# Optimization experiments

Measured on AMD Instinct MI355X. Metric: run time of the kernel, lower is better.

## Reference

```python
import jax, jax.numpy as jnp
import numpy as np
from jax import lax

V, E, T, F, K = 100000, 300, 50, 100, 3
B, S = 32, 512


def setup_inputs() -> dict:
    key = jax.random.key(0)
    ks = jax.random.split(key, 10)
    inp = {
        "x": jax.random.randint(ks[0], (B, S), 0, V),
        "tags": jax.random.randint(ks[1], (B, S), 0, T),
        "emb": jax.random.normal(ks[2], (V, E), dtype=jnp.float32),
        "conv_w": jax.random.normal(ks[3], (F, E, K), dtype=jnp.float32) / np.sqrt(E * K),
        "conv_b": jnp.zeros((F,), dtype=jnp.float32),
        "fc_w": jax.random.normal(ks[4], (T, F), dtype=jnp.float32) / np.sqrt(F),
        "fc_b": jnp.zeros((T,), dtype=jnp.float32),
        "start_trans": jax.random.uniform(ks[5], (T,), dtype=jnp.float32, minval=-0.1, maxval=0.1),
        "end_trans": jax.random.uniform(ks[6], (T,), dtype=jnp.float32, minval=-0.1, maxval=0.1),
        "trans": jax.random.uniform(ks[7], (T, T), dtype=jnp.float32, minval=-0.1, maxval=0.1),
    }
    return inp


def _emissions(x, emb, conv_w, conv_b, fc_w, fc_b):
    e = emb[x]                                   # [B,S,E] embedding gather
    e = jnp.transpose(e, (0, 2, 1))              # [B,E,S]
    h = lax.conv_general_dilated(e, conv_w, (1,), [(K // 2, K // 2)])  # [B,F,S] (NCW/OIW)
    h = jax.nn.relu(h + conv_b[None, :, None])   # dropout is identity in eval
    feat = jnp.transpose(h, (0, 2, 1))           # [B,S,F]
    return (jnp.einsum("bsf,tf->bst", feat, fc_w) + fc_b).astype(jnp.float32)  # [B,S,T]


def _crf_nll(emissions, tags, start_trans, end_trans, trans):
    # numerator: score of the gold tag path (full mask)
    em_tag = jnp.take_along_axis(emissions, tags[..., None], axis=-1)[..., 0]  # [B,S]
    num = (start_trans[tags[:, 0]]
           + em_tag.sum(-1)
           + trans[tags[:, :-1], tags[:, 1:]].sum(-1)
           + end_trans[tags[:, -1]])                                           # [B]

    # denominator: forward algorithm via scan over time
    alpha0 = start_trans[None, :] + emissions[:, 0]                             # [B,T]

    def step(alpha, em_t):
        # alpha: [B,T] prev scores; em_t: [B,T] emissions at t
        new = jax.nn.logsumexp(alpha[:, :, None] + trans[None] + em_t[:, None, :], axis=1)
        return new, None

    alpha, _ = lax.scan(step, alpha0, jnp.transpose(emissions[:, 1:], (1, 0, 2)))
    log_z = jax.nn.logsumexp(alpha + end_trans[None, :], axis=-1)               # [B]
    return -(num - log_z).sum()  # torchcrf default reduction='sum'; model returns -llh


def reference(x, tags, emb, conv_w, conv_b, fc_w, fc_b, start_trans, end_trans, trans):
    emissions = _emissions(x, emb, conv_w, conv_b, fc_w, fc_b)
    return _crf_nll(emissions, tags, start_trans, end_trans, trans)
```

## Files before the change

kernel.cpp:

```cpp
#include <hip/hip_runtime.h>
#include <hip/hip_bf16.h>
#include <math.h>

#define BB 32
#define SS 512
#define EE 300
#define FF 100
#define TT 50
#define CH 16
#define NC 32

typedef __attribute__((ext_vector_type(8))) short v8s;
typedef __attribute__((ext_vector_type(4))) float v4f;
#define MFMA16 __builtin_amdgcn_mfma_f32_16x16x32_bf16

#define AP 328
#define NCH 10
#define CKS 3
#define CHB (128 * 96)
#define A2P 136
#define MP 72

__device__ inline unsigned short f2bf(float v) {
    unsigned u = __float_as_uint(v);
    unsigned r = u + 0x7fff + ((u >> 16) & 1);
    return (unsigned short)(r >> 16);
}
__device__ inline float bf2f(short s) {
    return __uint_as_float(((unsigned)(unsigned short)s) << 16);
}
__device__ inline unsigned pkbf2(float a, float b) {
    __hip_bfloat162 h = __float22bfloat162_rn(make_float2(a, b));
    return *(unsigned*)&h;
}
__device__ inline v8s ldsld8(const short* p) {
    return *(const v8s*)__builtin_assume_aligned(p, 16);
}
__device__ inline void g2lds16(const void* g, void* l) {
    __builtin_amdgcn_global_load_lds(
        (const __attribute__((address_space(1))) unsigned int*)g,
        (__attribute__((address_space(3))) unsigned int*)l, 16, 0, 0);
}

__global__ void prep_kernel(const float* __restrict__ tr, const float* __restrict__ cw,
                            const float* __restrict__ fcw,
                            unsigned short* __restrict__ wB2,
                            unsigned short* __restrict__ fcwT2,
                            unsigned short* __restrict__ AT,
                            unsigned short* __restrict__ Ab,
                            float* __restrict__ accum, unsigned* __restrict__ cnt)
{
    const int gid = blockIdx.x * 256 + threadIdx.x;
    const int gs  = 64 * 256;
    if (gid == 0) { *accum = 0.f; *cnt = 0u; }
    for (int idx = gid; idx < NCH * CKS * 8 * 512; idx += gs) {
        int e = idx & 7, p = (idx >> 3) & 63, blk = idx >> 9;
        int ch = blk / 24, rem = blk - ch * 24;
        int sl = rem >> 3, ft = rem & 7;
        int col = p >> 2, q = p & 3;
        int n  = ft * 16 + col;
        int gk = ch * 96 + sl * 32 + q * 8 + e;
        int kk = gk / 320, ee = gk - kk * 320;
        float v = (n < FF && ee < EE) ? cw[n * 900 + ee * 3 + kk] : 0.f;
        wB2[idx] = f2bf(v);
    }
    for (int idx = gid; idx < 16 * 512; idx += gs) {
        int e = idx & 7, p = (idx >> 3) & 63, blk = idx >> 9;
        int ks = blk >> 2, nt = blk & 3;
        int col = p >> 2, q = p & 3;
        int t = nt * 16 + col, f = ks * 32 + q * 8 + e;
        float v = (t < TT && f < FF) ? fcw[t * FF + f] : 0.f;
        fcwT2[idx] = f2bf(v);
    }
    for (int idx = gid; idx < 64 * 64; idx += gs) {
        int r = idx >> 6, c2 = idx & 63;
        AT[idx] = (r < TT && c2 < TT) ? f2bf(__expf(tr[c2 * TT + r])) : 0;
        Ab[idx] = (r < TT && c2 < TT) ? f2bf(__expf(tr[r * TT + c2])) : 0;
    }
}

__global__ __launch_bounds__(256, 3) void emis_kernel(
    const int* __restrict__ x, const float* __restrict__ emb,
    const unsigned short* __restrict__ wB2, const float* __restrict__ cb,
    const unsigned short* __restrict__ fcwT2, const float* __restrict__ fcb,
    const int* __restrict__ tags,
    float* __restrict__ expem, float* __restrict__ rmv, float* __restrict__ emtag)
{
    __shared__ __align__(16) short ldsA[34 * AP];
    __shared__ __align__(16) short ldsB[CHB];

    const int b    = blockIdx.y;
    const int s0   = blockIdx.x * 32;
    const int tid  = threadIdx.x;
    const int wv   = tid >> 6;
    const int lane = tid & 63;
    const int col  = lane & 15;
    const int q    = lane >> 4;
    const int bofs = ((col << 2) | q) << 3;

#pragma unroll
    for (int it = 0; it < 6; ++it) {
        int seg = it * 4 + wv;
        g2lds16((const char*)wB2 + seg * 1024 + lane * 16,
                (char*)ldsB + seg * 1024);
    }

    int   xr[10], ofs[10], e0a[10];
#pragma unroll
    for (int it = 0; it < 10; ++it) {
        int g = tid + it * 256;
        int r = g / 75, eg = g - r * 75;
        int e0 = eg * 4;
        int src = s0 - 1 + r;
        bool v = (g < 2550) && (src >= 0) && (src < SS);
        xr[it]  = v ? x[b * SS + src] : -1;
        ofs[it] = r * AP + e0;
        e0a[it] = e0;
    }
    float4 vv[10];
#pragma unroll
    for (int it = 0; it < 10; ++it)
        vv[it] = (xr[it] >= 0)
               ? *(const float4*)(emb + (size_t)xr[it] * EE + e0a[it])
               : make_float4(0.f, 0.f, 0.f, 0.f);
#pragma unroll
    for (int it = 0; it < 10; ++it) {
        int g = tid + it * 256;
        if (g < 2550) {
            unsigned lo = pkbf2(vv[it].x, vv[it].y);
            unsigned hi = pkbf2(vv[it].z, vv[it].w);
            *(uint2*)&ldsA[ofs[it]] = make_uint2(lo, hi);
        }
    }
    if (tid < 34 * 5) {
        int r = tid / 5, c0 = 300 + (tid % 5) * 4;
        *(short4*)&ldsA[r * AP + c0] = make_short4(0, 0, 0, 0);
    }

    v4f acc[2][2];
#pragma unroll
    for (int a = 0; a < 2; ++a)
#pragma unroll
        for (int f = 0; f < 2; ++f) acc[a][f] = (v4f){0.f, 0.f, 0.f, 0.f};

    const int ftA = wv * 2, ftB = wv * 2 + 1;
    for (int ch = 0; ch < NCH; ++ch) {
        __syncthreads();
#pragma unroll
        for (int sl = 0; sl < CKS; ++sl) {
            int gk = ch * 96 + sl * 32;
            int kk = (gk >= 640) ? 2 : (gk >= 320 ? 1 : 0);
            int e0 = gk - kk * 320;
            v8s a0 = ldsld8(&ldsA[(col + kk) * AP + e0 + q * 8]);
            v8s a1 = ldsld8(&ldsA[(16 + col + kk) * AP + e0 + q * 8]);
            v8s b0 = ldsld8(&ldsB[((sl * 8 + ftA) << 9) + bofs]);
            v8s b1 = ldsld8(&ldsB[((sl * 8 + ftB) << 9) + bofs]);
            acc[0][0] = MFMA16(a0, b0, acc[0][0], 0, 0, 0);
            acc[0][1] = MFMA16(a0, b1, acc[0][1], 0, 0, 0);
            acc[1][0] = MFMA16(a1, b0, acc[1][0], 0, 0, 0);
            acc[1][1] = MFMA16(a1, b1, acc[1][1], 0, 0, 0);
        }
        __syncthreads();
        if (ch < NCH - 1) {
            const char* g = (const char*)(wB2 + (size_t)(ch + 1) * CHB);
#pragma unroll
            for (int it = 0; it < 6; ++it) {
                int seg = it * 4 + wv;
                g2lds16(g + seg * 1024 + lane * 16, (char*)ldsB + seg * 1024);
            }
        }
    }

    short* A2 = ldsA;
    short* B2 = ldsB;
#pragma unroll
    for (int it = 0; it < 4; ++it) {
        int seg = it * 4 + wv;
        g2lds16((const char*)fcwT2 + seg * 1024 + lane * 16,
                (char*)B2 + seg * 1024);
    }
#pragma unroll
    for (int st = 0; st < 2; ++st)
#pragma unroll
        for (int fi = 0; fi < 2; ++fi) {
            int f = (wv * 2 + fi) * 16 + col;
            float bias = (f < FF) ? cb[f] : 0.f;
#pragma unroll
            for (int rg = 0; rg < 4; ++rg) {
                int s = st * 16 + q * 4 + rg;
                float v = (f < FF) ? fmaxf(acc[st][fi][rg] + bias, 0.f) : 0.f;
                A2[s * A2P + f] = (short)f2bf(v);
            }
        }
    __syncthreads();

    if (wv < 2) {
        v4f a2[4];
#pragma unroll
        for (int nt = 0; nt < 4; ++nt) a2[nt] = (v4f){0.f, 0.f, 0.f, 0.f};
#pragma unroll
        for (int ks = 0; ks < 4; ++ks) {
            v8s af = ldsld8(&A2[(wv * 16 + col) * A2P + ks * 32 + q * 8]);
#pragma unroll
            for (int nt = 0; nt < 4; ++nt) {
                v8s bt = ldsld8(&B2[((ks * 4 + nt) << 9) + bofs]);
                a2[nt] = MFMA16(af, bt, a2[nt], 0, 0, 0);
            }
        }
        float fb0 = fcb[col], fb1 = fcb[16 + col], fb2 = fcb[32 + col];
        float fb3 = (col < 2) ? fcb[48 + col] : 0.f;
#pragma unroll
        for (int rg = 0; rg < 4; ++rg) {
            int s = s0 + wv * 16 + q * 4 + rg;
            float e0v = a2[0][rg] + fb0;
            float e1v = a2[1][rg] + fb1;
            float e2v = a2[2][rg] + fb2;
            float e3v = (col < 2) ? a2[3][rg] + fb3 : -1e30f;
            float m = fmaxf(fmaxf(e0v, e1v), fmaxf(e2v, e3v));
#pragma unroll
            for (int off = 1; off < 16; off <<= 1) m = fmaxf(m, __shfl_xor(m, off));
            int gidx = b * SS + s;
            if (col == 0) rmv[gidx] = m;
            int tg = tags[gidx];
            float* orow = expem + (size_t)gidx * TT;
            orow[col]      = __expf(e0v - m);
            orow[16 + col] = __expf(e1v - m);
            orow[32 + col] = __expf(e2v - m);
            if (col < 2) orow[48 + col] = __expf(e3v - m);
            if (tg == col)            emtag[gidx] = e0v;
            else if (tg == 16 + col)  emtag[gidx] = e1v;
            else if (tg == 32 + col)  emtag[gidx] = e2v;
            else if (col < 2 && tg == 48 + col) emtag[gidx] = e3v;
        }
    }
}

__global__ __launch_bounds__(64) void chunk_kernel(
    const float* __restrict__ expem, const unsigned short* __restrict__ AT,
    const unsigned short* __restrict__ Ab,
    unsigned short* __restrict__ R, float* __restrict__ lsR)
{
    __shared__ __align__(16) short L[2][64 * MP];
    __shared__ __align__(16) float emL[CH][64];
    const int c = blockIdx.x, b = blockIdx.y;
    const int lane = threadIdx.x;
    const int col = lane & 15, q = lane >> 4;
    const int t0 = c * CH + 1;
    const int nf = (c == NC - 1) ? (SS - 1 - (NC - 1) * CH) : CH;

    for (int idx = lane; idx < CH * 64; idx += 64) {
        int k = idx >> 6, m = idx & 63;
        float v = 0.f;
        if (m < TT && k < nf) v = expem[((size_t)(b * SS + t0 + k)) * TT + m];
        emL[k][m] = v;
    }

    v8s af[4][2];
#pragma unroll
    for (int jt = 0; jt < 4; ++jt)
#pragma unroll
        for (int kc = 0; kc < 2; ++kc)
            af[jt][kc] = *(const v8s*)(AT + (jt * 16 + col) * 64 + kc * 32 + q * 8);
    __syncthreads();

    {
        const v8s* arow = (const v8s*)(Ab + lane * 64);
#pragma unroll
        for (int g = 0; g < 8; ++g) {
            v8s a = arow[g];
            float f[8];
#pragma unroll
            for (int e = 0; e < 8; ++e) f[e] = bf2f(a[e]) * emL[0][g * 8 + e];
            uint4 o = make_uint4(pkbf2(f[0], f[1]), pkbf2(f[2], f[3]),
                                 pkbf2(f[4], f[5]), pkbf2(f[6], f[7]));
            *(uint4*)&L[0][lane * MP + g * 8] = o;
        }
    }

    int cur = 0;
    for (int k = 1; k < nf; ++k) {
        __syncthreads();
        v8s bf[4][2];
#pragma unroll
        for (int nt = 0; nt < 4; ++nt)
#pragma unroll
            for (int kc = 0; kc < 2; ++kc)
                bf[nt][kc] = ldsld8(&L[cur][(nt * 16 + col) * MP + kc * 32 + q * 8]);
        v4f acc[4][4];
#pragma unroll
        for (int jt = 0; jt < 4; ++jt)
#pragma unroll
            for (int nt = 0; nt < 4; ++nt) {
                acc[jt][nt] = (v4f){0.f, 0.f, 0.f, 0.f};
                acc[jt][nt] = MFMA16(af[jt][0], bf[nt][0], acc[jt][nt], 0, 0, 0);
                acc[jt][nt] = MFMA16(af[jt][1], bf[nt][1], acc[jt][nt], 0, 0, 0);
            }
        if (k < nf - 1) {
#pragma unroll
            for (int jt = 0; jt < 4; ++jt) {
                const float4 em4 = *(const float4*)&emL[k][jt * 16 + q * 4];
#pragma unroll
                for (int nt = 0; nt < 4; ++nt) {
                    uint2 o = make_uint2(
                        pkbf2(acc[jt][nt][0] * em4.x, acc[jt][nt][1] * em4.y),
                        pkbf2(acc[jt][nt][2] * em4.z, acc[jt][nt][3] * em4.w));
                    *(uint2*)&L[cur ^ 1][(nt * 16 + col) * MP + jt * 16 + q * 4] = o;
                }
            }
            cur ^= 1;
        } else {
            float vals[4][4][4];
            float mx = 0.f;
#pragma unroll
            for (int jt = 0; jt < 4; ++jt) {
                const float4 em4 = *(const float4*)&emL[k][jt * 16 + q * 4];
#pragma unroll
                for (int nt = 0; nt < 4; ++nt) {
                    vals[jt][nt][0] = acc[jt][nt][0] * em4.x;
                    vals[jt][nt][1] = acc[jt][nt][1] * em4.y;
                    vals[jt][nt][2] = acc[jt][nt][2] * em4.z;
                    vals[jt][nt][3] = acc[jt][nt][3] * em4.w;
#pragma unroll
                    for (int r = 0; r < 4; ++r) mx = fmaxf(mx, vals[jt][nt][r]);
                }
            }
#pragma unroll
            for (int off = 1; off < 64; off <<= 1) mx = fmaxf(mx, __shfl_xor(mx, off));
            mx = fmaxf(mx, 1e-37f);
            float inv = 1.f / mx;
            unsigned short* Rc = R + ((size_t)(b * NC + c) << 12);
#pragma unroll
            for (int jt = 0; jt < 4; ++jt)
#pragma unroll
                for (int nt = 0; nt < 4; ++nt)
#pragma unroll
                    for (int r = 0; r < 4; ++r)
                        Rc[(jt * 16 + q * 4 + r) * 64 + nt * 16 + col] =
                            f2bf(vals[jt][nt][r] * inv);
            if (lane == 0) lsR[b * NC + c] = __logf(mx);
        }
    }
}

__global__ __launch_bounds__(256) void chain_kernel(
    const float* __restrict__ expem, const unsigned short* __restrict__ R,
    const float* __restrict__ lsR, const float* __restrict__ start,
    const float* __restrict__ endt,
    const float* __restrict__ emtag, const float* __restrict__ rmv,
    const int* __restrict__ tags, const float* __restrict__ tr,
    float* __restrict__ accum, unsigned* __restrict__ cnt,
    float* __restrict__ out)
{
    __shared__ __align__(16) float pvec[64];
    __shared__ float red[8];
    __shared__ float lzsh;
    const int b = blockIdx.x, tid = threadIdx.x;
    const int wv = tid >> 6, i = tid & 63;

    if (wv == 0) {
        pvec[i] = (i < TT) ? __expf(start[i]) * expem[((size_t)(b * SS)) * TT + i] : 0.f;
        const unsigned short* Rb = R + ((size_t)(b * NC) << 12);
        v8s rb[3][8];
#pragma unroll
        for (int pc = 0; pc < 3; ++pc)
#pragma unroll
            for (int g = 0; g < 8; ++g)
                rb[pc][g] = *(const v8s*)(Rb + ((size_t)pc << 12) + i * 64 + g * 8);
        float logacc = 0.f;
#pragma unroll
        for (int c = 0; c < NC; ++c) {
            const int slot = c % 3;
            float acc = 0.f;
            const float4* pv = (const float4*)pvec;
#pragma unroll
            for (int g = 0; g < 8; ++g) {
                v8s v = rb[slot][g];
                float4 pA = pv[g * 2], pB = pv[g * 2 + 1];
                acc = fmaf(bf2f(v[0]), pA.x, acc);
                acc = fmaf(bf2f(v[1]), pA.y, acc);
                acc = fmaf(bf2f(v[2]), pA.z, acc);
                acc = fmaf(bf2f(v[3]), pA.w, acc);
                acc = fmaf(bf2f(v[4]), pB.x, acc);
                acc = fmaf(bf2f(v[5]), pB.y, acc);
                acc = fmaf(bf2f(v[6]), pB.z, acc);
                acc = fmaf(bf2f(v[7]), pB.w, acc);
            }
            if (c + 3 < NC) {
                const unsigned short* Rn = Rb + ((size_t)(c + 3) << 12);
#pragma unroll
                for (int g = 0; g < 8; ++g)
                    rb[slot][g] = *(const v8s*)(Rn + i * 64 + g * 8);
            }
            float mx = acc;
#pragma unroll
            for (int off = 1; off < 64; off <<= 1) mx = fmaxf(mx, __shfl_xor(mx, off));
            mx = fmaxf(mx, 1e-37f);
            logacc += __logf(mx) + lsR[b * NC + c];
            pvec[i] = acc * (1.f / mx);
        }
        float sv = (i < TT) ? pvec[i] * __expf(endt[i]) : 0.f;
#pragma unroll
        for (int off = 1; off < 64; off <<= 1) sv += __shfl_xor(sv, off);
        if (i == 0) lzsh = logacc + __logf(sv);
    } else {
        float accN = 0.f, accR = 0.f;
        for (int s = tid - 64; s < SS; s += 192) {
            int gi = b * SS + s;
            accN += emtag[gi];
            accR += rmv[gi];
            int tg = tags[gi];
            if (s < SS - 1) accN += tr[tg * TT + tags[gi + 1]];
        }
#pragma unroll
        for (int off = 1; off < 64; off <<= 1) {
            accN += __shfl_xor(accN, off);
            accR += __shfl_xor(accR, off);
        }
        if (i == 0) { red[wv] = accN; red[4 + wv] = accR; }
    }
    __syncthreads();
    if (tid == 0) {
        float tn  = red[1] + red[2] + red[3];
        float trm = red[5] + red[6] + red[7];
        float num = tn + start[tags[b * SS]] + endt[tags[b * SS + SS - 1]];
        float nll = trm + lzsh - num;
        atomicAdd(accum, nll);
        __threadfence();
        unsigned old = atomicAdd(cnt, 1u);
        if (old == BB - 1) out[0] = atomicAdd(accum, 0.f);
    }
}

extern "C" void kernel_launch(void* const* d_in, const int* in_sizes, int n_in,
                              void* d_out, int out_size, void* d_ws, size_t ws_size,
                              hipStream_t stream)
{
    const int*   x    = (const int*)d_in[0];
    const int*   tags = (const int*)d_in[1];
    const float* emb  = (const float*)d_in[2];
    const float* cw   = (const float*)d_in[3];
    const float* cb   = (const float*)d_in[4];
    const float* fcw  = (const float*)d_in[5];
    const float* fcb  = (const float*)d_in[6];
    const float* st   = (const float*)d_in[7];
    const float* en   = (const float*)d_in[8];
    const float* tr   = (const float*)d_in[9];

    unsigned short* wB2   = (unsigned short*)d_ws;
    unsigned short* fcwT2 = wB2 + NCH * CKS * 8 * 512;
    unsigned short* ATm   = fcwT2 + 16 * 512;
    unsigned short* Abm   = ATm + 4096;
    unsigned short* Rm    = Abm + 4096;
    float* fbase   = (float*)(Rm + (size_t)BB * NC * 4096);
    float* expem   = fbase;
    float* rmv     = expem + (size_t)BB * SS * TT;
    float* emtag   = rmv + BB * SS;
    float* lsR     = emtag + BB * SS;
    float* accum   = lsR + BB * NC;
    unsigned* cnt  = (unsigned*)(accum + 1);

    prep_kernel<<<dim3(64), 256, 0, stream>>>(tr, cw, fcw, wB2, fcwT2, ATm, Abm,
                                              accum, cnt);
    emis_kernel<<<dim3(16, BB), 256, 0, stream>>>(x, emb, wB2, cb, fcwT2, fcb,
                                                  tags, expem, rmv, emtag);
    chunk_kernel<<<dim3(NC, BB), 64, 0, stream>>>(expem, ATm, Abm, Rm, lsR);
    chain_kernel<<<dim3(BB), 256, 0, stream>>>(expem, Rm, lsR, st, en,
                                               emtag, rmv, tags, tr,
                                               accum, cnt, (float*)d_out);
}
```

Measured before the change: 241.4 us.

## Fuse chunk and chain kernels via last-block detection; fold numerator into emission kernel

Merges the per-chunk transfer-matrix kernel and the sequential chain kernel into one launch. The last chunk block to finish for each batch, detected with a per-batch atomic counter, runs the forward-chain reduction. The gold-path numerator and the row-max correction are now summed into a per-batch partial inside the emission kernel, which removes the rmv/emtag buffers and their re-read. The chunk kernel also moves to two waves per block, each handling half the output rows, and the chain uses four-deep prefetch with split accumulators. This removes one launch and some global traffic, but adds atomics, fences and an extra barrier for the cross-wave max.

```diff
diff --git a/kernel.cpp b/kernel.cpp
--- a/kernel.cpp
+++ b/kernel.cpp
@@ -48,11 +48,13 @@
                             unsigned short* __restrict__ fcwT2,
                             unsigned short* __restrict__ AT,
                             unsigned short* __restrict__ Ab,
-                            float* __restrict__ accum, unsigned* __restrict__ cnt)
+                            float* __restrict__ accum, unsigned* __restrict__ cnt,
+                            float* __restrict__ nllpart, unsigned* __restrict__ doneb)
 {
     const int gid = blockIdx.x * 256 + threadIdx.x;
     const int gs  = 64 * 256;
     if (gid == 0) { *accum = 0.f; *cnt = 0u; }
+    if (gid < BB) { nllpart[gid] = 0.f; doneb[gid] = 0u; }
     for (int idx = gid; idx < NCH * CKS * 8 * 512; idx += gs) {
         int e = idx & 7, p = (idx >> 3) & 63, blk = idx >> 9;
         int ch = blk / 24, rem = blk - ch * 24;
@@ -83,11 +85,13 @@
     const int* __restrict__ x, const float* __restrict__ emb,
     const unsigned short* __restrict__ wB2, const float* __restrict__ cb,
     const unsigned short* __restrict__ fcwT2, const float* __restrict__ fcb,
-    const int* __restrict__ tags,
-    float* __restrict__ expem, float* __restrict__ rmv, float* __restrict__ emtag)
+    const int* __restrict__ tags, const float* __restrict__ tr,
+    const float* __restrict__ start, const float* __restrict__ endt,
+    float* __restrict__ expem, float* __restrict__ nllpart)
 {
     __shared__ __align__(16) short ldsA[34 * AP];
     __shared__ __align__(16) short ldsB[CHB];
+    __shared__ float redN[2];
 
     const int b    = blockIdx.y;
     const int s0   = blockIdx.x * 32;
@@ -209,6 +213,7 @@
         }
         float fb0 = fcb[col], fb1 = fcb[16 + col], fb2 = fcb[32 + col];
         float fb3 = (col < 2) ? fcb[48 + col] : 0.f;
+        float nllp = 0.f;
 #pragma unroll
         for (int rg = 0; rg < 4; ++rg) {
             int s = s0 + wv * 16 + q * 4 + rg;
@@ -220,60 +225,80 @@
 #pragma unroll
             for (int off = 1; off < 16; off <<= 1) m = fmaxf(m, __shfl_xor(m, off));
             int gidx = b * SS + s;
-            if (col == 0) rmv[gidx] = m;
             int tg = tags[gidx];
             float* orow = expem + (size_t)gidx * TT;
             orow[col]      = __expf(e0v - m);
             orow[16 + col] = __expf(e1v - m);
             orow[32 + col] = __expf(e2v - m);
             if (col < 2) orow[48 + col] = __expf(e3v - m);
-            if (tg == col)            emtag[gidx] = e0v;
-            else if (tg == 16 + col)  emtag[gidx] = e1v;
-            else if (tg == 32 + col)  emtag[gidx] = e2v;
-            else if (col < 2 && tg == 48 + col) emtag[gidx] = e3v;
-        }
-    }
-}
-
-__global__ __launch_bounds__(64) void chunk_kernel(
+            if (tg == col)            nllp -= e0v;
+            else if (tg == 16 + col)  nllp -= e1v;
+            else if (tg == 32 + col)  nllp -= e2v;
+            else if (col < 2 && tg == 48 + col) nllp -= e3v;
+            if (col == 0) {
+                nllp += m;
+                if (s < SS - 1) nllp -= tr[tg * TT + tags[gidx + 1]];
+                if (s == 0)      nllp -= start[tg];
+                if (s == SS - 1) nllp -= endt[tg];
+            }
+        }
+#pragma unroll
+        for (int off = 1; off < 64; off <<= 1) nllp += __shfl_xor(nllp, off);
+        if (lane == 0) redN[wv] = nllp;
+    }
+    __syncthreads();
+    if (tid == 0) atomicAdd(nllpart + b, redN[0] + redN[1]);
+}
+
+__global__ __launch_bounds__(128) void chunkchain_kernel(
     const float* __restrict__ expem, const unsigned short* __restrict__ AT,
     const unsigned short* __restrict__ Ab,
-    unsigned short* __restrict__ R, float* __restrict__ lsR)
+    unsigned short* __restrict__ R, float* __restrict__ lsR,
+    const float* __restrict__ start, const float* __restrict__ endt,
+    const float* __restrict__ nllpart, unsigned* __restrict__ doneb,
+    float* __restrict__ accum, unsigned* __restrict__ cnt,
+    float* __restrict__ out)
 {
     __shared__ __align__(16) short L[2][64 * MP];
     __shared__ __align__(16) float emL[CH][64];
+    __shared__ float mxsh[2];
+    __shared__ unsigned lastf;
     const int c = blockIdx.x, b = blockIdx.y;
-    const int lane = threadIdx.x;
+    const int tid  = threadIdx.x;
+    const int wv   = tid >> 6;
+    const int lane = tid & 63;
     const int col = lane & 15, q = lane >> 4;
     const int t0 = c * CH + 1;
     const int nf = (c == NC - 1) ? (SS - 1 - (NC - 1) * CH) : CH;
 
-    for (int idx = lane; idx < CH * 64; idx += 64) {
+    for (int idx = tid; idx < CH * 64; idx += 128) {
         int k = idx >> 6, m = idx & 63;
         float v = 0.f;
         if (m < TT && k < nf) v = expem[((size_t)(b * SS + t0 + k)) * TT + m];
         emL[k][m] = v;
     }
 
-    v8s af[4][2];
-#pragma unroll
-    for (int jt = 0; jt < 4; ++jt)
+    v8s af[2][2];
+#pragma unroll
+    for (int jl = 0; jl < 2; ++jl)
 #pragma unroll
         for (int kc = 0; kc < 2; ++kc)
-            af[jt][kc] = *(const v8s*)(AT + (jt * 16 + col) * 64 + kc * 32 + q * 8);
+            af[jl][kc] = *(const v8s*)(AT + ((wv * 2 + jl) * 16 + col) * 64 + kc * 32 + q * 8);
     __syncthreads();
 
     {
-        const v8s* arow = (const v8s*)(Ab + lane * 64);
-#pragma unroll
-        for (int g = 0; g < 8; ++g) {
+        const int row = tid >> 1, half = tid & 1;
+        const v8s* arow = (const v8s*)(Ab + row * 64);
+#pragma unroll
+        for (int gh = 0; gh < 4; ++gh) {
+            int g = half * 4 + gh;
             v8s a = arow[g];
             float f[8];
 #pragma unroll
             for (int e = 0; e < 8; ++e) f[e] = bf2f(a[e]) * emL[0][g * 8 + e];
             uint4 o = make_uint4(pkbf2(f[0], f[1]), pkbf2(f[2], f[3]),
                                  pkbf2(f[4], f[5]), pkbf2(f[6], f[7]));
-            *(uint4*)&L[0][lane * MP + g * 8] = o;
+            *(uint4*)&L[0][row * MP + g * 8] = o;
         }
     }
 
@@ -286,148 +311,130 @@
 #pragma unroll
             for (int kc = 0; kc < 2; ++kc)
                 bf[nt][kc] = ldsld8(&L[cur][(nt * 16 + col) * MP + kc * 32 + q * 8]);
-        v4f acc[4][4];
-#pragma unroll
-        for (int jt = 0; jt < 4; ++jt)
+        v4f acc[2][4];
+#pragma unroll
+        for (int jl = 0; jl < 2; ++jl)
 #pragma unroll
             for (int nt = 0; nt < 4; ++nt) {
-                acc[jt][nt] = (v4f){0.f, 0.f, 0.f, 0.f};
-                acc[jt][nt] = MFMA16(af[jt][0], bf[nt][0], acc[jt][nt], 0, 0, 0);
-                acc[jt][nt] = MFMA16(af[jt][1], bf[nt][1], acc[jt][nt], 0, 0, 0);
+                acc[jl][nt] = (v4f){0.f, 0.f, 0.f, 0.f};
+                acc[jl][nt] = MFMA16(af[jl][0], bf[nt][0], acc[jl][nt], 0, 0, 0);
+                acc[jl][nt] = MFMA16(af[jl][1], bf[nt][1], acc[jl][nt], 0, 0, 0);
             }
         if (k < nf - 1) {
 #pragma unroll
-            for (int jt = 0; jt < 4; ++jt) {
+            for (int jl = 0; jl < 2; ++jl) {
+                const int jt = wv * 2 + jl;
                 const float4 em4 = *(const float4*)&emL[k][jt * 16 + q * 4];
 #pragma unroll
                 for (int nt = 0; nt < 4; ++nt) {
                     uint2 o = make_uint2(
-                        pkbf2(acc[jt][nt][0] * em4.x, acc[jt][nt][1] * em4.y),
-                        pkbf2(acc[jt][nt][2] * em4.z, acc[jt][nt][3] * em4.w));
+                        pkbf2(acc[jl][nt][0] * em4.x, acc[jl][nt][1] * em4.y),
+                        pkbf2(acc[jl][nt][2] * em4.z, acc[jl][nt][3] * em4.w));
                     *(uint2*)&L[cur ^ 1][(nt * 16 + col) * MP + jt * 16 + q * 4] = o;
                 }
             }
             cur ^= 1;
         } else {
-            float vals[4][4][4];
+            float vals[2][4][4];
             float mx = 0.f;
 #pragma unroll
-            for (int jt = 0; jt < 4; ++jt) {
+            for (int jl = 0; jl < 2; ++jl) {
+                const int jt = wv * 2 + jl;
                 const float4 em4 = *(const float4*)&emL[k][jt * 16 + q * 4];
 #pragma unroll
                 for (int nt = 0; nt < 4; ++nt) {
-                    vals[jt][nt][0] = acc[jt][nt][0] * em4.x;
-                    vals[jt][nt][1] = acc[jt][nt][1] * em4.y;
-                    vals[jt][nt][2] = acc[jt][nt][2] * em4.z;
-                    vals[jt][nt][3] = acc[jt][nt][3] * em4.w;
-#pragma unroll
-                    for (int r = 0; r < 4; ++r) mx = fmaxf(mx, vals[jt][nt][r]);
+                    vals[jl][nt][0] = acc[jl][nt][0] * em4.x;
+                    vals[jl][nt][1] = acc[jl][nt][1] * em4.y;
+                    vals[jl][nt][2] = acc[jl][nt][2] * em4.z;
+                    vals[jl][nt][3] = acc[jl][nt][3] * em4.w;
+#pragma unroll
+                    for (int r = 0; r < 4; ++r) mx = fmaxf(mx, vals[jl][nt][r]);
                 }
             }
 #pragma unroll
             for (int off = 1; off < 64; off <<= 1) mx = fmaxf(mx, __shfl_xor(mx, off));
-            mx = fmaxf(mx, 1e-37f);
+            if (lane == 0) mxsh[wv] = mx;
+            __syncthreads();
+            mx = fmaxf(fmaxf(mxsh[0], mxsh[1]), 1e-37f);
             float inv = 1.f / mx;
             unsigned short* Rc = R + ((size_t)(b * NC + c) << 12);
 #pragma unroll
-            for (int jt = 0; jt < 4; ++jt)
+            for (int jl = 0; jl < 2; ++jl)
 #pragma unroll
                 for (int nt = 0; nt < 4; ++nt)
 #pragma unroll
                     for (int r = 0; r < 4; ++r)
-                        Rc[(jt * 16 + q * 4 + r) * 64 + nt * 16 + col] =
-                            f2bf(vals[jt][nt][r] * inv);
-            if (lane == 0) lsR[b * NC + c] = __logf(mx);
-        }
-    }
-}
-
-__global__ __launch_bounds__(256) void chain_kernel(
-    const float* __restrict__ expem, const unsigned short* __restrict__ R,
-    const float* __restrict__ lsR, const float* __restrict__ start,
-    const float* __restrict__ endt,
-    const float* __restrict__ emtag, const float* __restrict__ rmv,
-    const int* __restrict__ tags, const float* __restrict__ tr,
-    float* __restrict__ accum, unsigned* __restrict__ cnt,
-    float* __restrict__ out)
-{
-    __shared__ __align__(16) float pvec[64];
-    __shared__ float red[8];
-    __shared__ float lzsh;
-    const int b = blockIdx.x, tid = threadIdx.x;
-    const int wv = tid >> 6, i = tid & 63;
-
-    if (wv == 0) {
-        pvec[i] = (i < TT) ? __expf(start[i]) * expem[((size_t)(b * SS)) * TT + i] : 0.f;
-        const unsigned short* Rb = R + ((size_t)(b * NC) << 12);
-        v8s rb[3][8];
-#pragma unroll
-        for (int pc = 0; pc < 3; ++pc)
-#pragma unroll
-            for (int g = 0; g < 8; ++g)
-                rb[pc][g] = *(const v8s*)(Rb + ((size_t)pc << 12) + i * 64 + g * 8);
-        float logacc = 0.f;
-#pragma unroll
-        for (int c = 0; c < NC; ++c) {
-            const int slot = c % 3;
-            float acc = 0.f;
-            const float4* pv = (const float4*)pvec;
-#pragma unroll
-            for (int g = 0; g < 8; ++g) {
-                v8s v = rb[slot][g];
-                float4 pA = pv[g * 2], pB = pv[g * 2 + 1];
-                acc = fmaf(bf2f(v[0]), pA.x, acc);
-                acc = fmaf(bf2f(v[1]), pA.y, acc);
-                acc = fmaf(bf2f(v[2]), pA.z, acc);
-                acc = fmaf(bf2f(v[3]), pA.w, acc);
-                acc = fmaf(bf2f(v[4]), pB.x, acc);
-                acc = fmaf(bf2f(v[5]), pB.y, acc);
-                acc = fmaf(bf2f(v[6]), pB.z, acc);
-                acc = fmaf(bf2f(v[7]), pB.w, acc);
-            }
-            if (c + 3 < NC) {
-                const unsigned short* Rn = Rb + ((size_t)(c + 3) << 12);
-#pragma unroll
-                for (int g = 0; g < 8; ++g)
-                    rb[slot][g] = *(const v8s*)(Rn + i * 64 + g * 8);
-            }
-            float mx = acc;
-#pragma unroll
-            for (int off = 1; off < 64; off <<= 1) mx = fmaxf(mx, __shfl_xor(mx, off));
-            mx = fmaxf(mx, 1e-37f);
-            logacc += __logf(mx) + lsR[b * NC + c];
-            pvec[i] = acc * (1.f / mx);
-        }
-        float sv = (i < TT) ? pvec[i] * __expf(endt[i]) : 0.f;
-#pragma unroll
-        for (int off = 1; off < 64; off <<= 1) sv += __shfl_xor(sv, off);
-        if (i == 0) lzsh = logacc + __logf(sv);
-    } else {
-        float accN = 0.f, accR = 0.f;
-        for (int s = tid - 64; s < SS; s += 192) {
-            int gi = b * SS + s;
-            accN += emtag[gi];
-            accR += rmv[gi];
-            int tg = tags[gi];
-            if (s < SS - 1) accN += tr[tg * TT + tags[gi + 1]];
-        }
-#pragma unroll
-        for (int off = 1; off < 64; off <<= 1) {
-            accN += __shfl_xor(accN, off);
-            accR += __shfl_xor(accR, off);
-        }
-        if (i == 0) { red[wv] = accN; red[4 + wv] = accR; }
-    }
+                        Rc[((wv * 2 + jl) * 16 + q * 4 + r) * 64 + nt * 16 + col] =
+                            f2bf(vals[jl][nt][r] * inv);
+            if (tid == 0) lsR[b * NC + c] = __logf(mx);
+        }
+    }
+
     __syncthreads();
     if (tid == 0) {
-        float tn  = red[1] + red[2] + red[3];
-        float trm = red[5] + red[6] + red[7];
-        float num = tn + start[tags[b * SS]] + endt[tags[b * SS + SS - 1]];
-        float nll = trm + lzsh - num;
+        __threadfence();
+        unsigned o = atomicAdd(doneb + b, 1u);
+        lastf = (o == NC - 1) ? 1u : 0u;
+    }
+    __syncthreads();
+    if (!lastf || wv != 0) return;
+
+    __threadfence();
+    const int i = lane;
+    float* pvec = &emL[0][0];
+    pvec[i] = (i < TT) ? __expf(start[i]) * expem[((size_t)(b * SS)) * TT + i] : 0.f;
+    const unsigned short* Rb = R + ((size_t)(b * NC) << 12);
+    v8s rb[4][8];
+#pragma unroll
+    for (int pc = 0; pc < 4; ++pc)
+#pragma unroll
+        for (int g = 0; g < 8; ++g)
+            rb[pc][g] = *(const v8s*)(Rb + ((size_t)pc << 12) + i * 64 + g * 8);
+    float logacc = 0.f;
+#pragma unroll
+    for (int cc = 0; cc < NC; ++cc) {
+        const int slot = cc & 3;
+        const float4* pv4 = (const float4*)pvec;
+        float a0 = 0.f, a1 = 0.f, a2 = 0.f, a3 = 0.f;
+#pragma unroll
+        for (int g = 0; g < 8; ++g) {
+            v8s v = rb[slot][g];
+            float4 pA = pv4[g * 2], pB = pv4[g * 2 + 1];
+            float* aa = (g & 3) == 0 ? &a0 : (g & 3) == 1 ? &a1 : (g & 3) == 2 ? &a2 : &a3;
+            float t = *aa;
+            t = fmaf(bf2f(v[0]), pA.x, t);
+            t = fmaf(bf2f(v[1]), pA.y, t);
+            t = fmaf(bf2f(v[2]), pA.z, t);
+            t = fmaf(bf2f(v[3]), pA.w, t);
+            t = fmaf(bf2f(v[4]), pB.x, t);
+            t = fmaf(bf2f(v[5]), pB.y, t);
+            t = fmaf(bf2f(v[6]), pB.z, t);
+            t = fmaf(bf2f(v[7]), pB.w, t);
+            *aa = t;
+        }
+        float acc2 = (a0 + a1) + (a2 + a3);
+        if (cc + 4 < NC) {
+            const unsigned short* Rn = Rb + ((size_t)(cc + 4) << 12);
+#pragma unroll
+            for (int g = 0; g < 8; ++g)
+                rb[slot][g] = *(const v8s*)(Rn + i * 64 + g * 8);
+        }
+        float mx = acc2;
+#pragma unroll
+        for (int off = 1; off < 64; off <<= 1) mx = fmaxf(mx, __shfl_xor(mx, off));
+        mx = fmaxf(mx, 1e-37f);
+        logacc += __logf(mx) + lsR[b * NC + cc];
+        pvec[i] = acc2 * (1.f / mx);
+    }
+    float sv = (i < TT) ? pvec[i] * __expf(endt[i]) : 0.f;
+#pragma unroll
+    for (int off = 1; off < 64; off <<= 1) sv += __shfl_xor(sv, off);
+    if (i == 0) {
+        float nll = nllpart[b] + logacc + __logf(sv);
         atomicAdd(accum, nll);
         __threadfence();
-        unsigned old = atomicAdd(cnt, 1u);
-        if (old == BB - 1) out[0] = atomicAdd(accum, 0.f);
+        unsigned o = atomicAdd(cnt, 1u);
+        if (o == BB - 1) out[0] = atomicAdd(accum, 0.f);
     }
 }
 
@@ -453,18 +460,17 @@
     unsigned short* Rm    = Abm + 4096;
     float* fbase   = (float*)(Rm + (size_t)BB * NC * 4096);
     float* expem   = fbase;
-    float* rmv     = expem + (size_t)BB * SS * TT;
-    float* emtag   = rmv + BB * SS;
-    float* lsR     = emtag + BB * SS;
-    float* accum   = lsR + BB * NC;
+    float* lsR     = expem + (size_t)BB * SS * TT;
+    float* nllpart = lsR + BB * NC;
+    float* accum   = nllpart + BB;
     unsigned* cnt  = (unsigned*)(accum + 1);
+    unsigned* doneb = cnt + 1;
 
     prep_kernel<<<dim3(64), 256, 0, stream>>>(tr, cw, fcw, wB2, fcwT2, ATm, Abm,
-                                              accum, cnt);
+                                              accum, cnt, nllpart, doneb);
     emis_kernel<<<dim3(16, BB), 256, 0, stream>>>(x, emb, wB2, cb, fcwT2, fcb,
-                                                  tags, expem, rmv, emtag);
-    chunk_kernel<<<dim3(NC, BB), 64, 0, stream>>>(expem, ATm, Abm, Rm, lsR);
-    chain_kernel<<<dim3(BB), 256, 0, stream>>>(expem, Rm, lsR, st, en,
-                                               emtag, rmv, tags, tr,
-                                               accum, cnt, (float*)d_out);
-}
+                                                  tags, tr, st, en, expem, nllpart);
+    chunkchain_kernel<<<dim3(NC, BB), 128, 0, stream>>>(expem, ATm, Abm, Rm, lsR,
+                                                        st, en, nllpart, doneb,
+                                                        accum, cnt, (float*)d_out);
+}
```

Result: slower. 283.6 us (+17.5%).

## Double-buffer conv weight chunks in LDS and restructure CRF chain loop

Applied to the files above, without the earlier changes.

The emission kernel now double-buffers the conv weight chunks in LDS. The next chunk is prefetched before the current chunk's MFMAs run, which removes one barrier per chunk, and the fc weight load is folded into the last iteration. This doubles the LDS footprint for B and lowers the launch-bounds occupancy hint from 3 to 2 blocks. The chain kernel replaces its fully unrolled 3-slot prefetch with a two-buffer ping-pong loop, splits each dot product across four accumulators to shorten the dependency chain, and reduces the lsR log-scales once up front instead of per step.

```diff
diff --git a/kernel.cpp b/kernel.cpp
--- a/kernel.cpp
+++ b/kernel.cpp
@@ -79,7 +79,7 @@
     }
 }
 
-__global__ __launch_bounds__(256, 3) void emis_kernel(
+__global__ __launch_bounds__(256, 2) void emis_kernel(
     const int* __restrict__ x, const float* __restrict__ emb,
     const unsigned short* __restrict__ wB2, const float* __restrict__ cb,
     const unsigned short* __restrict__ fcwT2, const float* __restrict__ fcb,
@@ -87,7 +87,7 @@
     float* __restrict__ expem, float* __restrict__ rmv, float* __restrict__ emtag)
 {
     __shared__ __align__(16) short ldsA[34 * AP];
-    __shared__ __align__(16) short ldsB[CHB];
+    __shared__ __align__(16) short ldsB[2 * CHB];
 
     const int b    = blockIdx.y;
     const int s0   = blockIdx.x * 32;
@@ -146,6 +146,23 @@
     const int ftA = wv * 2, ftB = wv * 2 + 1;
     for (int ch = 0; ch < NCH; ++ch) {
         __syncthreads();
+        if (ch < NCH - 1) {
+            const char* g = (const char*)(wB2 + (size_t)(ch + 1) * CHB);
+            char* l = (char*)ldsB + ((ch + 1) & 1) * (CHB * 2);
+#pragma unroll
+            for (int it = 0; it < 6; ++it) {
+                int seg = it * 4 + wv;
+                g2lds16(g + seg * 1024 + lane * 16, l + seg * 1024);
+            }
+        } else {
+#pragma unroll
+            for (int it = 0; it < 4; ++it) {
+                int seg = it * 4 + wv;
+                g2lds16((const char*)fcwT2 + seg * 1024 + lane * 16,
+                        (char*)ldsB + seg * 1024);
+            }
+        }
+        const short* Bc = ldsB + (ch & 1) * CHB;
 #pragma unroll
         for (int sl = 0; sl < CKS; ++sl) {
             int gk = ch * 96 + sl * 32;
@@ -153,32 +170,18 @@
             int e0 = gk - kk * 320;
             v8s a0 = ldsld8(&ldsA[(col + kk) * AP + e0 + q * 8]);
             v8s a1 = ldsld8(&ldsA[(16 + col + kk) * AP + e0 + q * 8]);
-            v8s b0 = ldsld8(&ldsB[((sl * 8 + ftA) << 9) + bofs]);
-            v8s b1 = ldsld8(&ldsB[((sl * 8 + ftB) << 9) + bofs]);
+            v8s b0 = ldsld8(&Bc[((sl * 8 + ftA) << 9) + bofs]);
+            v8s b1 = ldsld8(&Bc[((sl * 8 + ftB) << 9) + bofs]);
             acc[0][0] = MFMA16(a0, b0, acc[0][0], 0, 0, 0);
             acc[0][1] = MFMA16(a0, b1, acc[0][1], 0, 0, 0);
             acc[1][0] = MFMA16(a1, b0, acc[1][0], 0, 0, 0);
             acc[1][1] = MFMA16(a1, b1, acc[1][1], 0, 0, 0);
         }
-        __syncthreads();
-        if (ch < NCH - 1) {
-            const char* g = (const char*)(wB2 + (size_t)(ch + 1) * CHB);
-#pragma unroll
-            for (int it = 0; it < 6; ++it) {
-                int seg = it * 4 + wv;
-                g2lds16(g + seg * 1024 + lane * 16, (char*)ldsB + seg * 1024);
-            }
-        }
-    }
+    }
+    __syncthreads();
 
     short* A2 = ldsA;
     short* B2 = ldsB;
-#pragma unroll
-    for (int it = 0; it < 4; ++it) {
-        int seg = it * 4 + wv;
-        g2lds16((const char*)fcwT2 + seg * 1024 + lane * 16,
-                (char*)B2 + seg * 1024);
-    }
 #pragma unroll
     for (int st = 0; st < 2; ++st)
 #pragma unroll
@@ -340,6 +343,37 @@
             if (lane == 0) lsR[b * NC + c] = __logf(mx);
         }
     }
+}
+
+__device__ inline float chaindot(const v8s (&buf)[8], const float* pvec) {
+    const float4* pv4 = (const float4*)__builtin_assume_aligned(pvec, 16);
+    float a0 = 0.f, a1 = 0.f, a2 = 0.f, a3 = 0.f;
+#pragma unroll
+    for (int g = 0; g < 8; ++g) {
+        v8s v = buf[g];
+        float4 pA = pv4[g * 2], pB = pv4[g * 2 + 1];
+        float* aa = (g & 3) == 0 ? &a0 : (g & 3) == 1 ? &a1 : (g & 3) == 2 ? &a2 : &a3;
+        float t = *aa;
+        t = fmaf(bf2f(v[0]), pA.x, t);
+        t = fmaf(bf2f(v[1]), pA.y, t);
+        t = fmaf(bf2f(v[2]), pA.z, t);
+        t = fmaf(bf2f(v[3]), pA.w, t);
+        t = fmaf(bf2f(v[4]), pB.x, t);
+        t = fmaf(bf2f(v[5]), pB.y, t);
+        t = fmaf(bf2f(v[6]), pB.z, t);
+        t = fmaf(bf2f(v[7]), pB.w, t);
+        *aa = t;
+    }
+    return (a0 + a1) + (a2 + a3);
+}
+
+__device__ inline void chainfin(float acc2, float* pvec, int i, float& logacc) {
+    float mx = acc2;
+#pragma unroll
+    for (int off = 1; off < 64; off <<= 1) mx = fmaxf(mx, __shfl_xor(mx, off));
+    mx = fmaxf(mx, 1e-37f);
+    logacc += __logf(mx);
+    pvec[i] = acc2 * (1.f / mx);
 }
 
 __global__ __launch_bounds__(256) void chain_kernel(
@@ -359,49 +393,37 @@
 
     if (wv == 0) {
         pvec[i] = (i < TT) ? __expf(start[i]) * expem[((size_t)(b * SS)) * TT + i] : 0.f;
+        float lsv = (i < NC) ? lsR[b * NC + i] : 0.f;
+#pragma unroll
+        for (int off = 1; off < 64; off <<= 1) lsv += __shfl_xor(lsv, off);
+
         const unsigned short* Rb = R + ((size_t)(b * NC) << 12);
-        v8s rb[3][8];
-#pragma unroll
-        for (int pc = 0; pc < 3; ++pc)
+        v8s bufA[8], bufB[8];
+#pragma unroll
+        for (int g = 0; g < 8; ++g)
+            bufA[g] = *(const v8s*)(Rb + i * 64 + g * 8);
+        float logacc = 0.f;
+#pragma unroll 1
+        for (int cc = 0; cc < NC; cc += 2) {
+            const unsigned short* R1 = Rb + ((size_t)(cc + 1) << 12);
 #pragma unroll
             for (int g = 0; g < 8; ++g)
-                rb[pc][g] = *(const v8s*)(Rb + ((size_t)pc << 12) + i * 64 + g * 8);
-        float logacc = 0.f;
-#pragma unroll
-        for (int c = 0; c < NC; ++c) {
-            const int slot = c % 3;
-            float acc = 0.f;
-            const float4* pv = (const float4*)pvec;
-#pragma unroll
-            for (int g = 0; g < 8; ++g) {
-                v8s v = rb[slot][g];
-                float4 pA = pv[g * 2], pB = pv[g * 2 + 1];
-                acc = fmaf(bf2f(v[0]), pA.x, acc);
-                acc = fmaf(bf2f(v[1]), pA.y, acc);
-                acc = fmaf(bf2f(v[2]), pA.z, acc);
-                acc = fmaf(bf2f(v[3]), pA.w, acc);
-                acc = fmaf(bf2f(v[4]), pB.x, acc);
-                acc = fmaf(bf2f(v[5]), pB.y, acc);
-                acc = fmaf(bf2f(v[6]), pB.z, acc);
-                acc = fmaf(bf2f(v[7]), pB.w, acc);
-            }
-            if (c + 3 < NC) {
-                const unsigned short* Rn = Rb + ((size_t)(c + 3) << 12);
+                bufB[g] = *(const v8s*)(R1 + i * 64 + g * 8);
+            float acc2 = chaindot(bufA, pvec);
+            chainfin(acc2, pvec, i, logacc);
+            if (cc + 2 < NC) {
+                const unsigned short* R2 = Rb + ((size_t)(cc + 2) << 12);
 #pragma unroll
                 for (int g = 0; g < 8; ++g)
-                    rb[slot][g] = *(const v8s*)(Rn + i * 64 + g * 8);
-            }
-            float mx = acc;
-#pragma unroll
-            for (int off = 1; off < 64; off <<= 1) mx = fmaxf(mx, __shfl_xor(mx, off));
-            mx = fmaxf(mx, 1e-37f);
-            logacc += __logf(mx) + lsR[b * NC + c];
-            pvec[i] = acc * (1.f / mx);
+                    bufA[g] = *(const v8s*)(R2 + i * 64 + g * 8);
+            }
+            acc2 = chaindot(bufB, pvec);
+            chainfin(acc2, pvec, i, logacc);
         }
         float sv = (i < TT) ? pvec[i] * __expf(endt[i]) : 0.f;
 #pragma unroll
         for (int off = 1; off < 64; off <<= 1) sv += __shfl_xor(sv, off);
-        if (i == 0) lzsh = logacc + __logf(sv);
+        if (i == 0) lzsh = logacc + lsv + __logf(sv);
     } else {
         float accN = 0.f, accR = 0.f;
         for (int s = tid - 64; s < SS; s += 192) {
```

Measured after the change: 239.7 us. No clear change (-0.7%).
